# Performance work log

Hardware: AMD Instinct MI355X
Metric: run time of the kernel (lower is better)

Reference implementation:

```python
import jax, jax.numpy as jnp
import numpy as np

N_SEG = 65536          # number of output segments
TOTAL = 2097152        # total input rows (avg 32 per segment)
D = 128                # feature dim


def setup_inputs() -> dict:
    key = jax.random.key(0)
    kx, kp = jax.random.split(key)
    x = jax.random.normal(kx, (TOTAL, D), dtype=jnp.float32)
    # CSR indptr: sorted random interior boundaries, endpoints pinned to 0 and TOTAL
    inner = jnp.sort(jax.random.randint(kp, (N_SEG - 1,), 0, TOTAL, dtype=jnp.int64))
    indptr = jnp.concatenate([
        jnp.zeros((1,), dtype=jnp.int64),
        inner,
        jnp.full((1,), TOTAL, dtype=jnp.int64),
    ])  # [N_SEG + 1]
    return {"x": x, "indptr": indptr}


def _indptr_to_segment_ids(indptr, total):
    # Marker-and-cumsum: handles empty segments (duplicate indptr values) via .add
    marks = jnp.zeros((total,), dtype=jnp.int32)
    marks = marks.at[indptr[1:-1]].add(1)
    return jnp.cumsum(marks)  # [total] segment id per row


def reference(x, indptr):
    # segment_csr(x, indptr, reduce='sum'): out[i] = sum of x[indptr[i]:indptr[i+1]]
    seg_ids = _indptr_to_segment_ids(indptr, x.shape[0])
    return jax.ops.segment_sum(x, seg_ids, num_segments=N_SEG)  # [N_SEG, D]
```

## Files before the change

kernel.cpp:

```cpp
#include <hip/hip_runtime.h>


#define NSEG 65536
#define D4   32

__global__ __launch_bounds__(256) void segcsr_kernel(
    const float4* __restrict__ x,
    const int*    __restrict__ indptr,
    float4*       __restrict__ out)
{
    const int seg  = (blockIdx.x << 2) + (threadIdx.x >> 6);
    const int lane = threadIdx.x & 63;
    const int c    = lane & 31;
    const int rh   = lane >> 5;

    const int begin = indptr[seg];
    const int end   = indptr[seg + 1];

    float ax = 0.f, ay = 0.f, az = 0.f, aw = 0.f;
    for (int r = begin + rh; r < end; r += 2) {
        const float4 v = x[(long long)r * D4 + c];
        ax += v.x; ay += v.y; az += v.z; aw += v.w;
    }

    ax += __shfl_down(ax, 32);
    ay += __shfl_down(ay, 32);
    az += __shfl_down(az, 32);
    aw += __shfl_down(aw, 32);

    if (rh == 0) {
        float4 o; o.x = ax; o.y = ay; o.z = az; o.w = aw;
        out[(long long)seg * D4 + c] = o;
    }
}

extern "C" void kernel_launch(void* const* d_in, const int* in_sizes, int n_in,
                              void* d_out, int out_size, void* d_ws, size_t ws_size,
                              hipStream_t stream) {
    const float4* x      = (const float4*)d_in[0];
    const int*    indptr = (const int*)d_in[1];
    float4*       out    = (float4*)d_out;

    dim3 grid(NSEG / 4), block(256);
    segcsr_kernel<<<grid, block, 0, stream>>>(x, indptr, out);
}
```

Before: 1.367 ms.

## Replace per-segment reduction with fixed-row sweep using binary search and atomics

Each wavefront now sweeps a fixed chunk of 128 rows instead of handling one segment. It binary-searches indptr to find its starting segment, then streams rows with unrolled nontemporal loads. Segments that lie wholly inside a chunk are written directly, and segments that cross a chunk boundary are combined with atomicAdd. A separate kernel zeroes the output first so empty and partial segments come out right. The aim is to balance load despite uneven segment lengths and keep more loads in flight, at the cost of an extra zeroing pass, atomics, and a serial per-row boundary check.

```diff
diff --git a/kernel.cpp b/kernel.cpp
--- a/kernel.cpp
+++ b/kernel.cpp
@@ -1,46 +1,87 @@
 #include <hip/hip_runtime.h>
 
 
-#define NSEG 65536
-#define D4   32
+#define NSEG  65536
+#define TOTAL 2097152
+#define RPW   128
+#define UNR   8
 
-__global__ __launch_bounds__(256) void segcsr_kernel(
-    const float4* __restrict__ x,
-    const int*    __restrict__ indptr,
-    float4*       __restrict__ out)
+typedef float f32x2 __attribute__((ext_vector_type(2)));
+typedef float f32x4 __attribute__((ext_vector_type(4)));
+
+__global__ __launch_bounds__(256) void zero_out_kernel(f32x4* __restrict__ out4)
 {
-    const int seg  = (blockIdx.x << 2) + (threadIdx.x >> 6);
+    const size_t i = (size_t)blockIdx.x * 256 + threadIdx.x;
+    f32x4 z = {0.f, 0.f, 0.f, 0.f};
+    __builtin_nontemporal_store(z, out4 + i);
+}
+
+__global__ __launch_bounds__(256) void segcsr_sweep(
+    const f32x2* __restrict__ x,
+    const int*   __restrict__ indptr,
+    float*       __restrict__ out)
+{
+    const int wid  = __builtin_amdgcn_readfirstlane((blockIdx.x << 2) + (threadIdx.x >> 6));
     const int lane = threadIdx.x & 63;
-    const int c    = lane & 31;
-    const int rh   = lane >> 5;
+    const int r0 = wid * RPW;
+    const int r1 = r0 + RPW;
 
-    const int begin = indptr[seg];
-    const int end   = indptr[seg + 1];
+    int lo = 0, hi = NSEG;
+    while (hi - lo > 1) {
+        const int mid = (lo + hi) >> 1;
+        if (indptr[mid] <= r0) lo = mid; else hi = mid;
+    }
+    int s        = lo;
+    int segBegin = indptr[s];
+    int segEnd   = indptr[s + 1];
 
-    float ax = 0.f, ay = 0.f, az = 0.f, aw = 0.f;
-    for (int r = begin + rh; r < end; r += 2) {
-        const float4 v = x[(long long)r * D4 + c];
-        ax += v.x; ay += v.y; az += v.z; aw += v.w;
+    float ax = 0.f, ay = 0.f;
+    int lastFlush = r0;
+
+    for (int base = r0; base < r1; base += UNR) {
+        f32x2 v[UNR];
+#pragma unroll
+        for (int j = 0; j < UNR; ++j)
+            v[j] = __builtin_nontemporal_load(&x[(size_t)(base + j) * 64 + lane]);
+#pragma unroll
+        for (int j = 0; j < UNR; ++j) {
+            ax += v[j].x;
+            ay += v[j].y;
+            const int rr = base + j + 1;
+            if (rr == segEnd) {
+                float* o = out + (size_t)s * 128 + lane * 2;
+                if (segBegin >= r0) {
+                    o[0] = ax; o[1] = ay;
+                } else {
+                    atomicAdd(o,     ax);
+                    atomicAdd(o + 1, ay);
+                }
+                ax = 0.f; ay = 0.f;
+                lastFlush = rr;
+                if (rr < TOTAL) {
+                    do { s++; } while (indptr[s + 1] <= rr);
+                    segBegin = rr;
+                    segEnd   = indptr[s + 1];
+                }
+            }
+        }
     }
 
-    ax += __shfl_down(ax, 32);
-    ay += __shfl_down(ay, 32);
-    az += __shfl_down(az, 32);
-    aw += __shfl_down(aw, 32);
-
-    if (rh == 0) {
-        float4 o; o.x = ax; o.y = ay; o.z = az; o.w = aw;
-        out[(long long)seg * D4 + c] = o;
+    if (lastFlush < r1) {
+        float* o = out + (size_t)s * 128 + lane * 2;
+        atomicAdd(o,     ax);
+        atomicAdd(o + 1, ay);
     }
 }
 
 extern "C" void kernel_launch(void* const* d_in, const int* in_sizes, int n_in,
                               void* d_out, int out_size, void* d_ws, size_t ws_size,
                               hipStream_t stream) {
-    const float4* x      = (const float4*)d_in[0];
-    const int*    indptr = (const int*)d_in[1];
-    float4*       out    = (float4*)d_out;
+    const f32x2* x      = (const f32x2*)d_in[0];
+    const int*   indptr = (const int*)d_in[1];
+    float*       out    = (float*)d_out;
 
-    dim3 grid(NSEG / 4), block(256);
-    segcsr_kernel<<<grid, block, 0, stream>>>(x, indptr, out);
+    zero_out_kernel<<<dim3(8192), dim3(256), 0, stream>>>((f32x4*)out);
+
+    segcsr_sweep<<<dim3(TOTAL / RPW / 4), dim3(256), 0, stream>>>(x, indptr, out);
 }
```

Result: no change. 1.372 ms (+0.4%).
